# Kernel tuning notes

Measured on AMD Instinct MI355X. Metric: run time of the kernel, lower is better.

The kernel has to match this reference:

```python
import jax, jax.numpy as jnp
import numpy as np

HID = 1024
NH = 16
DH = HID // NH  # 64


def _heads(x):
    # [B, S, H] -> [B, nH, S, dh]
    B, S, _ = x.shape
    return x.reshape(B, S, NH, DH).transpose(0, 2, 1, 3)


def setup_inputs() -> dict:
    key = jax.random.key(0)
    ks = jax.random.split(key, 16)
    inp = {
        "word_hidden_states": jax.random.normal(ks[0], (2, 2048, HID), jnp.float32),
        "entity_hidden_states": jax.random.normal(ks[1], (2, 256, HID), jnp.float32),
    }
    scale = 1.0 / np.sqrt(HID)
    names = ["Wq", "Wk", "Wv", "Ww2e", "We2w", "We2e"]
    for i, n in enumerate(names):
        inp[n] = jax.random.normal(ks[2 + i], (HID, HID), jnp.float32) * scale
        inp["b" + n[1:]] = jnp.zeros((HID,), jnp.float32)
    return inp


def reference(word_hidden_states, entity_hidden_states,
              Wq, bq, Wk, bk, Wv, bv,
              Ww2e, bw2e, We2w, be2w, We2e, be2e):
    word, ent = word_hidden_states, entity_hidden_states
    B, Sw, _ = word.shape
    Se = ent.shape[1]
    hs = jnp.concatenate([word, ent], axis=1)  # [B, Sw+Se, H]

    # four query types, heads: [B, nH, S*, dh]
    q_w2w = _heads(word @ Wq + bq)
    q_w2e = _heads(word @ Ww2e + bw2e)
    q_e2w = _heads(ent @ We2w + be2w)
    q_e2e = _heads(ent @ We2e + be2e)

    k = _heads(hs @ Wk + bk)
    v = _heads(hs @ Wv + bv)
    k_w, k_e = k[:, :, :Sw, :], k[:, :, Sw:, :]

    # block scores
    s_w2w = jnp.einsum("bhqd,bhkd->bhqk", q_w2w, k_w)  # [B,nH,Sw,Sw]
    s_w2e = jnp.einsum("bhqd,bhkd->bhqk", q_w2e, k_e)  # [B,nH,Sw,Se]
    s_e2w = jnp.einsum("bhqd,bhkd->bhqk", q_e2w, k_w)  # [B,nH,Se,Sw]
    s_e2e = jnp.einsum("bhqd,bhkd->bhqk", q_e2e, k_e)  # [B,nH,Se,Se]

    word_scores = jnp.concatenate([s_w2w, s_w2e], axis=3)
    ent_scores = jnp.concatenate([s_e2w, s_e2e], axis=3)
    scores = jnp.concatenate([word_scores, ent_scores], axis=2)  # [B,nH,S,S]
    scores = scores / np.sqrt(DH)

    probs = jax.nn.softmax(scores, axis=-1)  # dropout is identity in eval
    ctx = jnp.einsum("bhqk,bhkd->bhqd", probs, v)  # [B,nH,S,dh]
    ctx = ctx.transpose(0, 2, 1, 3).reshape(B, Sw + Se, HID)
    return ctx[:, :Sw, :], ctx[:, Sw:, :]
```

## Files before the change

kernel.cpp:

```cpp
#include <hip/hip_runtime.h>
#include <hip/hip_bf16.h>

typedef __attribute__((ext_vector_type(8))) short short8;
typedef __attribute__((ext_vector_type(4))) float f32x4;
typedef __attribute__((ext_vector_type(16))) float f32x16;
typedef __attribute__((ext_vector_type(4))) unsigned short u16x4;
typedef __attribute__((ext_vector_type(8))) unsigned short u16x8;
typedef __attribute__((ext_vector_type(4))) unsigned int u32x4;

__device__ __forceinline__ unsigned short f2b(float f) {
  __hip_bfloat16 h = __float2bfloat16(f);
  return __builtin_bit_cast(unsigned short, h);
}

__device__ __forceinline__ float b2f(unsigned short u) {
  return __builtin_bit_cast(float, (unsigned int)u << 16);
}

__device__ __forceinline__ void gload_lds16(const void* g, void* l) {
  __builtin_amdgcn_global_load_lds(
      (const __attribute__((address_space(1))) unsigned int*)g,
      (__attribute__((address_space(3))) unsigned int*)l, 16, 0, 0);
}

__device__ __forceinline__ f32x16 mfma32(short8 a, short8 b, f32x16 c) {
  return __builtin_amdgcn_mfma_f32_32x32x16_bf16(a, b, c, 0, 0, 0);
}

__device__ __forceinline__ unsigned int cvtpk(float a, float b) {
  unsigned int r;
  asm("v_cvt_pk_bf16_f32 %0, %1, %2" : "=v"(r) : "v"(a), "v"(b));
  return r;
}

struct PrepassParams {
  const float* sw;
  const float* se;
  unsigned short* dw;
  unsigned short* de;
  const float* w[6];
  unsigned short* wt[6];
};

__global__ __launch_bounds__(256) void prepass(PrepassParams p) {
  const int bx = blockIdx.x;
  const int tid = threadIdx.x;
  if (bx < 2304) {
    int i = bx * 256 + tid;
    const float* s;
    unsigned short* d;
    int j;
    if (i < 524288) {
      s = p.sw; d = p.dw; j = i;
    } else {
      s = p.se; d = p.de; j = i - 524288;
      if (j >= 65536) return;
    }
    const f32x4* sp = (const f32x4*)s;
    f32x4 a = sp[2 * j];
    f32x4 b = sp[2 * j + 1];
    u16x8 o;
    o[0] = f2b(a[0]); o[1] = f2b(a[1]); o[2] = f2b(a[2]); o[3] = f2b(a[3]);
    o[4] = f2b(b[0]); o[5] = f2b(b[1]); o[6] = f2b(b[2]); o[7] = f2b(b[3]);
    ((u16x8*)d)[j] = o;
  } else {
    __shared__ float t[32][33];
    const int idx = bx - 2304;
    const int z = idx >> 10;
    const int rem = idx & 1023;
    const int bxx = rem & 31;
    const int byy = rem >> 5;
    const float* W = p.w[z];
    unsigned short* Wt = p.wt[z];
    const int tx = tid & 31, ty = tid >> 5;
#pragma unroll
    for (int i = 0; i < 4; ++i)
      t[ty + 8 * i][tx] = W[(byy * 32 + ty + 8 * i) * 1024 + bxx * 32 + tx];
    __syncthreads();
#pragma unroll
    for (int i = 0; i < 4; ++i)
      Wt[(bxx * 32 + ty + 8 * i) * 1024 + byy * 32 + tx] = f2b(t[tx][ty + 8 * i]);
  }
}

struct GemmJob {
  const unsigned short* Wt;
  const float* bias;
  unsigned short* out;
  int S;
  int s_off;
  int sshift;
  int trans;
  float scale;
};
struct Gemm2Params {
  const unsigned short* Aw;
  const unsigned short* Ae;
  GemmJob job[8];
};

__global__ __launch_bounds__(256) void gemm_qkv(Gemm2Params p) {
  __shared__ unsigned short smem[16384];
  unsigned short* As = smem;
  unsigned short* Bs = smem + 8192;
  const int tid = threadIdx.x;
  const int w = tid >> 6, lane = tid & 63;
  const int c = lane & 15, g = lane >> 4;
  const int wid = blockIdx.y + 36 * blockIdx.z;
  const int z = wid & 3;
  const int y = wid >> 2;
  const bool isword = y < 32;
  const GemmJob j = p.job[isword ? z : z + 4];
  const unsigned short* A = isword ? p.Aw : p.Ae;
  const long arow0 = (long)(isword ? y : y - 32) * 128;
  const unsigned short* B = j.Wt;
  const long brow0 = (long)blockIdx.x * 128;

  f32x4 acc[4][4] = {};

  for (int kt = 0; kt < 16; ++kt) {
    __syncthreads();
#pragma unroll
    for (int i = 0; i < 4; ++i) {
      int ch = i * 256 + tid;
      int row = ch >> 3;
      int k8 = ((ch & 7) ^ (row & 7)) << 3;
      const unsigned short* ga = A + (arow0 + row) * 1024 + kt * 64 + k8;
      const unsigned short* gb = B + (brow0 + row) * 1024 + kt * 64 + k8;
      gload_lds16(ga, As + (i * 256 + w * 64) * 8);
      gload_lds16(gb, Bs + (i * 256 + w * 64) * 8);
    }
    __syncthreads();
#pragma unroll
    for (int kf = 0; kf < 2; ++kf) {
      short8 av[4], bv[4];
#pragma unroll
      for (int mf = 0; mf < 4; ++mf) {
        int row = (w >> 1) * 64 + mf * 16 + c;
        int byte = (row * 128 + (kf * 32 + g * 8) * 2) ^ ((row & 7) << 4);
        av[mf] = *(const short8*)((const char*)As + byte);
      }
#pragma unroll
      for (int nf = 0; nf < 4; ++nf) {
        int row = (w & 1) * 64 + nf * 16 + c;
        int byte = (row * 128 + (kf * 32 + g * 8) * 2) ^ ((row & 7) << 4);
        bv[nf] = *(const short8*)((const char*)Bs + byte);
      }
      __builtin_amdgcn_s_setprio(1);
#pragma unroll
      for (int mf = 0; mf < 4; ++mf)
#pragma unroll
        for (int nf = 0; nf < 4; ++nf)
          acc[mf][nf] = __builtin_amdgcn_mfma_f32_16x16x32_bf16(av[mf], bv[nf],
                                                                acc[mf][nf], 0, 0, 0);
      __builtin_amdgcn_s_setprio(0);
    }
  }

  float biasv[4];
#pragma unroll
  for (int nf = 0; nf < 4; ++nf) {
    int n = (int)brow0 + (w & 1) * 64 + nf * 16 + c;
    biasv[nf] = j.bias[n];
  }
  const int smask = (1 << j.sshift) - 1;
  __syncthreads();

  if (j.trans) {
#pragma unroll
    for (int mf = 0; mf < 4; ++mf) {
      int m0 = (w >> 1) * 64 + mf * 16 + g * 4;
#pragma unroll
      for (int nf = 0; nf < 4; ++nf) {
        int n = (w & 1) * 64 + nf * 16 + c;
        u16x4 pv;
#pragma unroll
        for (int r = 0; r < 4; ++r)
          pv[r] = f2b((acc[mf][nf][r] + biasv[nf]) * j.scale);
        int byte = (n * 256 + m0 * 2) ^ ((n & 7) << 4);
        *(u16x4*)((char*)smem + byte) = pv;
      }
    }
    __syncthreads();
#pragma unroll
    for (int i = 0; i < 8; ++i) {
      int ch = i * 256 + tid;
      int nr = ch >> 4, sl = ch & 15;
      int byte = (nr * 256 + sl * 16) ^ ((nr & 7) << 4);
      u16x8 v = *(const u16x8*)((const char*)smem + byte);
      int n = (int)brow0 + nr;
      int hh = n >> 6, dd = n & 63;
      int m = (int)arow0 + sl * 8;
      int b_ = m >> j.sshift;
      int s = (m & smask) + j.s_off;
      *(u16x8*)(j.out + (((long)b_ * 16 + hh) * 64 + dd) * 2304 + s) = v;
    }
  } else {
#pragma unroll
    for (int mf = 0; mf < 4; ++mf) {
#pragma unroll
      for (int r = 0; r < 4; ++r) {
        int m = (w >> 1) * 64 + mf * 16 + g * 4 + r;
#pragma unroll
        for (int nf = 0; nf < 4; ++nf) {
          int n = (w & 1) * 64 + nf * 16 + c;
          unsigned short hv = f2b((acc[mf][nf][r] + biasv[nf]) * j.scale);
          int byte = (m * 256 + n * 2) ^ ((m & 7) << 4);
          *(unsigned short*)((char*)smem + byte) = hv;
        }
      }
    }
    __syncthreads();
#pragma unroll
    for (int i = 0; i < 8; ++i) {
      int ch = i * 256 + tid;
      int mr = ch >> 4, sl = ch & 15;
      int byte = (mr * 256 + sl * 16) ^ ((mr & 7) << 4);
      u16x8 v = *(const u16x8*)((const char*)smem + byte);
      int m = (int)arow0 + mr;
      int b_ = m >> j.sshift;
      int s = (m & smask) + j.s_off;
      int n = (int)brow0 + sl * 8;
      int hh = n >> 6, dd = n & 63;
      *(u16x8*)(j.out + (((long)b_ * 16 + hh) * j.S + s) * 64 + dd) = v;
    }
  }
}

__global__ __launch_bounds__(256) void attn_kernel(
    const unsigned short* __restrict__ qw2w, const unsigned short* __restrict__ qw2e,
    const unsigned short* __restrict__ qe2w, const unsigned short* __restrict__ qe2e,
    const unsigned short* __restrict__ Kg, const unsigned short* __restrict__ Vtg,
    unsigned short* __restrict__ po0, unsigned short* __restrict__ po1,
    float* __restrict__ lbuf) {
  __shared__ unsigned short smem[16384];

  const int tid = threadIdx.x;
  const int w = tid >> 6, lane = tid & 63;
  const int l31 = lane & 31, hf = lane >> 5;

  const int flat = blockIdx.x;
  const int work = (flat & 7) * 144 + (flat >> 3);
  const int part = work & 1;
  const int tile = (work % 36) >> 1;
  const int hb = work / 36;
  const int head = hb & 15, b = hb >> 4;

  const bool isw = tile < 16;
  const int Sq = isw ? 2048 : 256;
  const int q0 = (isw ? tile : tile - 16) * 128 + w * 32;
  const int bh = b * 16 + head;
  const unsigned short* Qa =
      (isw ? qw2w : qe2w) + ((long)bh * Sq + q0 + l31) * 64 + hf * 8;
  const unsigned short* Qb =
      (isw ? qw2e : qe2e) + ((long)bh * Sq + q0 + l31) * 64 + hf * 8;
  const unsigned short* Kb = Kg + (long)bh * 2304 * 64;
  const unsigned short* Vtb = Vtg + (long)bh * 64 * 2304;

  short8 qcur[4];
#pragma unroll
  for (int kf = 0; kf < 4; ++kf) qcur[kf] = *(const short8*)(Qa + kf * 16);

  f32x16 o[2] = {};
  float lrun = 0.f;

  auto stage = [&](int t, int bufi) {
    const unsigned short* Kt = Kb + t * 4096;
    unsigned short* Klp = smem + bufi * 4096;
    unsigned short* Vlp = smem + 8192 + bufi * 4096;
#pragma unroll
    for (int i = 0; i < 2; ++i) {
      int ch = i * 256 + tid;
      int row = ch >> 3, c8 = ch & 7;
      int col = (c8 ^ (row & 7)) << 3;
      gload_lds16(Kt + row * 64 + col, Klp + (i * 256 + (tid & 192)) * 8);
      gload_lds16(Vtb + row * 2304 + t * 64 + col, Vlp + (i * 256 + (tid & 192)) * 8);
    }
  };

  const int t0 = part * 18, t1 = t0 + 18;
  stage(t0, 0);
  int cur = 0;

  for (int t = t0; t < t1; ++t) {
    if (t == 32) {
#pragma unroll
      for (int kf = 0; kf < 4; ++kf) qcur[kf] = *(const short8*)(Qb + kf * 16);
    }
    if (t + 1 < t1) {
      stage(t + 1, cur ^ 1);
      asm volatile("s_waitcnt vmcnt(4)" ::: "memory");
    } else {
      asm volatile("s_waitcnt vmcnt(0)" ::: "memory");
    }
    __builtin_amdgcn_sched_barrier(0);
    __builtin_amdgcn_s_barrier();

    const char* Kbase = (const char*)(smem + cur * 4096);
    const char* Vbase = (const char*)(smem + 8192 + cur * 4096);

    f32x16 st[2] = {};
#pragma unroll
    for (int kg = 0; kg < 2; ++kg) {
      int row = kg * 32 + l31;
      int rb = (row * 128) | (hf * 16);
      int sw = (row & 7) << 4;
      short8 kfr[4];
#pragma unroll
      for (int kf = 0; kf < 4; ++kf)
        kfr[kf] = *(const short8*)(Kbase + ((rb + kf * 32) ^ sw));
      __builtin_amdgcn_s_setprio(1);
#pragma unroll
      for (int kf = 0; kf < 4; ++kf) st[kg] = mfma32(kfr[kf], qcur[kf], st[kg]);
      __builtin_amdgcn_s_setprio(0);
    }

    float s0 = 0.f, s1 = 0.f, s2 = 0.f, s3 = 0.f;
#pragma unroll
    for (int kg = 0; kg < 2; ++kg) {
#pragma unroll
      for (int r = 0; r < 16; r += 4) {
        float p0 = __builtin_amdgcn_exp2f(st[kg][r + 0]);
        float p1 = __builtin_amdgcn_exp2f(st[kg][r + 1]);
        float p2 = __builtin_amdgcn_exp2f(st[kg][r + 2]);
        float p3 = __builtin_amdgcn_exp2f(st[kg][r + 3]);
        st[kg][r + 0] = p0; st[kg][r + 1] = p1;
        st[kg][r + 2] = p2; st[kg][r + 3] = p3;
        s0 += p0; s1 += p1; s2 += p2; s3 += p3;
      }
    }
    lrun += (s0 + s1) + (s2 + s3);

#pragma unroll
    for (int kg = 0; kg < 2; ++kg)
#pragma unroll
      for (int hs = 0; hs < 2; ++hs) {
        const int rbase = hs * 8;
        unsigned int a0 = cvtpk(st[kg][rbase + 0], st[kg][rbase + 1]);
        unsigned int a1 = cvtpk(st[kg][rbase + 2], st[kg][rbase + 3]);
        unsigned int b0 = cvtpk(st[kg][rbase + 4], st[kg][rbase + 5]);
        unsigned int b1 = cvtpk(st[kg][rbase + 6], st[kg][rbase + 7]);
        asm("v_permlane32_swap_b32 %0, %1" : "+v"(a0), "+v"(b0));
        asm("v_permlane32_swap_b32 %0, %1" : "+v"(a1), "+v"(b1));
        u32x4 pw;
        pw[0] = a0; pw[1] = a1; pw[2] = b0; pw[3] = b1;
        short8 pf = __builtin_bit_cast(short8, pw);
        const int ks = kg * 2 + hs;
        short8 vf0, vf1;
        {
          int vrow = l31;
          int byte = ((vrow * 128) | (ks * 32 + hf * 16)) ^ ((vrow & 7) << 4);
          vf0 = *(const short8*)(Vbase + byte);
          vrow = 32 + l31;
          byte = ((vrow * 128) | (ks * 32 + hf * 16)) ^ ((vrow & 7) << 4);
          vf1 = *(const short8*)(Vbase + byte);
        }
        __builtin_amdgcn_s_setprio(1);
        o[0] = mfma32(vf0, pf, o[0]);
        o[1] = mfma32(vf1, pf, o[1]);
        __builtin_amdgcn_s_setprio(0);
      }

    asm volatile("s_waitcnt lgkmcnt(0)" ::: "memory");
    __builtin_amdgcn_sched_barrier(0);
    __builtin_amdgcn_s_barrier();
    cur ^= 1;
  }

  float ltot = lrun + __shfl_xor(lrun, 32);

  const int sgb = (isw ? 0 : 2048) + q0;
  if (hf == 0) lbuf[(long)part * 73728 + bh * 2304 + sgb + l31] = ltot;

  float* E = (float*)smem + w * 2048;
#pragma unroll
  for (int mf = 0; mf < 2; ++mf)
#pragma unroll
    for (int rg = 0; rg < 4; ++rg) {
      int d0 = mf * 32 + rg * 8 + hf * 4;
      f32x4 v;
      v[0] = o[mf][rg * 4 + 0];
      v[1] = o[mf][rg * 4 + 1];
      v[2] = o[mf][rg * 4 + 2];
      v[3] = o[mf][rg * 4 + 3];
      *(f32x4*)(E + l31 * 64 + (d0 ^ ((l31 & 7) << 2))) = v;
    }

  unsigned short* po = part ? po1 : po0;
  unsigned short* ob = isw
      ? po + (((long)b * 2048 + q0) * 1024 + head * 64)
      : po + (long)2 * 2048 * 1024 + (((long)b * 256 + q0) * 1024 + head * 64);
#pragma unroll
  for (int i = 0; i < 4; ++i) {
    int qr = (lane >> 3) + i * 8;
    int dcg = (lane & 7) * 8;
    int sw = (qr & 7) << 2;
    f32x4 v0 = *(const f32x4*)(E + qr * 64 + (dcg ^ sw));
    f32x4 v1 = *(const f32x4*)(E + qr * 64 + ((dcg + 4) ^ sw));
    u32x4 pk;
    pk[0] = cvtpk(v0[0], v0[1]);
    pk[1] = cvtpk(v0[2], v0[3]);
    pk[2] = cvtpk(v1[0], v1[1]);
    pk[3] = cvtpk(v1[2], v1[3]);
    *(u32x4*)(ob + (long)qr * 1024 + dcg) = pk;
  }
}

__global__ __launch_bounds__(256) void attn_merge(
    const unsigned short* __restrict__ po0, const unsigned short* __restrict__ po1,
    const float* __restrict__ lbuf, float* __restrict__ out) {
  long i = ((long)blockIdx.x * 256 + threadIdx.x) * 4;
  if (i >= 4718592) return;
  int bh, sg;
  if (i < 4194304) {
    int b = (int)(i >> 21), s = (int)((i >> 10) & 2047), h = (int)((i >> 6) & 15);
    bh = b * 16 + h;
    sg = s;
  } else {
    long j = i - 4194304;
    int b = (int)(j >> 18), s = (int)((j >> 10) & 255), h = (int)((j >> 6) & 15);
    bh = b * 16 + h;
    sg = 2048 + s;
  }
  float l0 = lbuf[bh * 2304 + sg];
  float l1 = lbuf[73728 + bh * 2304 + sg];
  u16x4 a4 = *(const u16x4*)(po0 + i);
  u16x4 c4 = *(const u16x4*)(po1 + i);
  float inv = 1.f / (l0 + l1);
  f32x4 r;
#pragma unroll
  for (int k = 0; k < 4; ++k) r[k] = (b2f(a4[k]) + b2f(c4[k])) * inv;
  *(f32x4*)(out + i) = r;
}

extern "C" void kernel_launch(void* const* d_in, const int* in_sizes, int n_in,
                              void* d_out, int out_size, void* d_ws, size_t ws_size,
                              hipStream_t stream) {
  (void)in_sizes; (void)n_in; (void)out_size; (void)ws_size;
  const float* word = (const float*)d_in[0];
  const float* ent = (const float*)d_in[1];

  char* ws = (char*)d_ws;
  size_t off = 0;
  auto alloc = [&](size_t bytes) {
    void* p = ws + off;
    off += (bytes + 255) & ~(size_t)255;
    return p;
  };
  unsigned short* Xw = (unsigned short*)alloc(4096ull * 1024 * 2);
  unsigned short* Xe = (unsigned short*)alloc(512ull * 1024 * 2);
  unsigned short* Wt[6];
  for (int i = 0; i < 6; ++i) Wt[i] = (unsigned short*)alloc(1024ull * 1024 * 2);
  unsigned short* qw2w = (unsigned short*)alloc(2ull * 16 * 2048 * 64 * 2);
  unsigned short* qw2e = (unsigned short*)alloc(2ull * 16 * 2048 * 64 * 2);
  unsigned short* qe2w = (unsigned short*)alloc(2ull * 16 * 256 * 64 * 2);
  unsigned short* qe2e = (unsigned short*)alloc(2ull * 16 * 256 * 64 * 2);
  unsigned short* Kbuf = (unsigned short*)alloc(2ull * 16 * 2304 * 64 * 2);
  unsigned short* Vtbuf = (unsigned short*)alloc(2ull * 16 * 64 * 2304 * 2);
  unsigned short* po1 = (unsigned short*)alloc(4718592ull * 2);
  float* lbuf = (float*)alloc(2ull * 73728 * 4);
  unsigned short* po0 = (unsigned short*)ws;

  PrepassParams pp;
  pp.sw = word;
  pp.se = ent;
  pp.dw = Xw;
  pp.de = Xe;
  pp.w[0] = (const float*)d_in[2];
  pp.w[1] = (const float*)d_in[4];
  pp.w[2] = (const float*)d_in[6];
  pp.w[3] = (const float*)d_in[8];
  pp.w[4] = (const float*)d_in[10];
  pp.w[5] = (const float*)d_in[12];
  for (int i = 0; i < 6; ++i) pp.wt[i] = Wt[i];
  prepass<<<8448, 256, 0, stream>>>(pp);

  const float* bq = (const float*)d_in[3];
  const float* bk = (const float*)d_in[5];
  const float* bv = (const float*)d_in[7];
  const float* bw2e = (const float*)d_in[9];
  const float* be2w = (const float*)d_in[11];
  const float* be2e = (const float*)d_in[13];
  const float qs = 0.125f * 1.44269504f;

  Gemm2Params gp;
  gp.Aw = Xw;
  gp.Ae = Xe;
  gp.job[0] = {Wt[0], bq, qw2w, 2048, 0, 11, 0, qs};
  gp.job[1] = {Wt[3], bw2e, qw2e, 2048, 0, 11, 0, qs};
  gp.job[2] = {Wt[1], bk, Kbuf, 2304, 0, 11, 0, 1.f};
  gp.job[3] = {Wt[2], bv, Vtbuf, 2304, 0, 11, 1, 1.f};
  gp.job[4] = {Wt[4], be2w, qe2w, 256, 0, 8, 0, qs};
  gp.job[5] = {Wt[5], be2e, qe2e, 256, 0, 8, 0, qs};
  gp.job[6] = {Wt[1], bk, Kbuf, 2304, 2048, 8, 0, 1.f};
  gp.job[7] = {Wt[2], bv, Vtbuf, 2304, 2048, 8, 1, 1.f};
  gemm_qkv<<<dim3(8, 36, 4), 256, 0, stream>>>(gp);

  attn_kernel<<<1152, 256, 0, stream>>>(qw2w, qw2e, qe2w, qe2e, Kbuf, Vtbuf,
                                        po0, po1, lbuf);
  attn_merge<<<4608, 256, 0, stream>>>(po0, po1, lbuf, (float*)d_out);
}
```

Before: 141.6 us.

## Fuse split-KV merge into attention kernel via per-pair atomic counter

```diff
diff --git a/kernel.cpp b/kernel.cpp
--- a/kernel.cpp
+++ b/kernel.cpp
@@ -40,11 +40,15 @@
   unsigned short* de;
   const float* w[6];
   unsigned short* wt[6];
+  int* cnt;
 };
 
 __global__ __launch_bounds__(256) void prepass(PrepassParams p) {
   const int bx = blockIdx.x;
   const int tid = threadIdx.x;
+  if (bx == 8447) {
+    for (int k = tid; k < 576; k += 256) p.cnt[k] = 0;
+  }
   if (bx < 2304) {
     int i = bx * 256 + tid;
     const float* s;
@@ -232,7 +236,7 @@
     const unsigned short* __restrict__ qe2w, const unsigned short* __restrict__ qe2e,
     const unsigned short* __restrict__ Kg, const unsigned short* __restrict__ Vtg,
     unsigned short* __restrict__ po0, unsigned short* __restrict__ po1,
-    float* __restrict__ lbuf) {
+    float* __restrict__ lbuf, int* __restrict__ cnt, float* __restrict__ out) {
   __shared__ unsigned short smem[16384];
 
   const int tid = threadIdx.x;
@@ -242,6 +246,7 @@
   const int flat = blockIdx.x;
   const int work = (flat & 7) * 144 + (flat >> 3);
   const int part = work & 1;
+  const int pair = work >> 1;
   const int tile = (work % 36) >> 1;
   const int hb = work / 36;
   const int head = hb & 15, b = hb >> 4;
@@ -386,10 +391,11 @@
       *(f32x4*)(E + l31 * 64 + (d0 ^ ((l31 & 7) << 2))) = v;
     }
 
-  unsigned short* po = part ? po1 : po0;
-  unsigned short* ob = isw
-      ? po + (((long)b * 2048 + q0) * 1024 + head * 64)
-      : po + (long)2 * 2048 * 1024 + (((long)b * 256 + q0) * 1024 + head * 64);
+  unsigned short* pself = part ? po1 : po0;
+  const long obase = isw ? (((long)b * 2048 + q0) * 1024 + head * 64)
+                         : (long)2 * 2048 * 1024 +
+                               (((long)b * 256 + q0) * 1024 + head * 64);
+  unsigned short* obs = pself + obase;
 #pragma unroll
   for (int i = 0; i < 4; ++i) {
     int qr = (lane >> 3) + i * 8;
@@ -402,35 +408,38 @@
     pk[1] = cvtpk(v0[2], v0[3]);
     pk[2] = cvtpk(v1[0], v1[1]);
     pk[3] = cvtpk(v1[2], v1[3]);
-    *(u32x4*)(ob + (long)qr * 1024 + dcg) = pk;
-  }
-}
-
-__global__ __launch_bounds__(256) void attn_merge(
-    const unsigned short* __restrict__ po0, const unsigned short* __restrict__ po1,
-    const float* __restrict__ lbuf, float* __restrict__ out) {
-  long i = ((long)blockIdx.x * 256 + threadIdx.x) * 4;
-  if (i >= 4718592) return;
-  int bh, sg;
-  if (i < 4194304) {
-    int b = (int)(i >> 21), s = (int)((i >> 10) & 2047), h = (int)((i >> 6) & 15);
-    bh = b * 16 + h;
-    sg = s;
-  } else {
-    long j = i - 4194304;
-    int b = (int)(j >> 18), s = (int)((j >> 10) & 255), h = (int)((j >> 6) & 15);
-    bh = b * 16 + h;
-    sg = 2048 + s;
-  }
-  float l0 = lbuf[bh * 2304 + sg];
-  float l1 = lbuf[73728 + bh * 2304 + sg];
-  u16x4 a4 = *(const u16x4*)(po0 + i);
-  u16x4 c4 = *(const u16x4*)(po1 + i);
-  float inv = 1.f / (l0 + l1);
-  f32x4 r;
-#pragma unroll
-  for (int k = 0; k < 4; ++k) r[k] = (b2f(a4[k]) + b2f(c4[k])) * inv;
-  *(f32x4*)(out + i) = r;
+    *(u32x4*)(obs + (long)qr * 1024 + dcg) = pk;
+  }
+
+  __threadfence();
+  __syncthreads();
+  __shared__ int flagLds;
+  if (tid == 0) flagLds = atomicAdd(&cnt[pair], 1);
+  __syncthreads();
+  if (flagLds == 1) {
+    const unsigned short* pother = part ? po0 : po1;
+    const unsigned short* obo = pother + obase;
+    float* oo = out + obase;
+    const float* lb0 = lbuf + bh * 2304 + sgb;
+    const float* lb1 = lbuf + 73728 + bh * 2304 + sgb;
+#pragma unroll
+    for (int i = 0; i < 4; ++i) {
+      int qr = (lane >> 3) + i * 8;
+      int dcg = (lane & 7) * 8;
+      long off = (long)qr * 1024 + dcg;
+      u16x8 a8 = *(const u16x8*)(obs + off);
+      u16x8 b8 = *(const u16x8*)(obo + off);
+      float inv = 1.f / (lb0[qr] + lb1[qr]);
+      f32x4 r0, r1;
+#pragma unroll
+      for (int k = 0; k < 4; ++k) {
+        r0[k] = (b2f(a8[k]) + b2f(b8[k])) * inv;
+        r1[k] = (b2f(a8[4 + k]) + b2f(b8[4 + k])) * inv;
+      }
+      *(f32x4*)(oo + off) = r0;
+      *(f32x4*)(oo + off + 4) = r1;
+    }
+  }
 }
 
 extern "C" void kernel_launch(void* const* d_in, const int* in_sizes, int n_in,
@@ -457,9 +466,10 @@
   unsigned short* qe2e = (unsigned short*)alloc(2ull * 16 * 256 * 64 * 2);
   unsigned short* Kbuf = (unsigned short*)alloc(2ull * 16 * 2304 * 64 * 2);
   unsigned short* Vtbuf = (unsigned short*)alloc(2ull * 16 * 64 * 2304 * 2);
+  unsigned short* po0 = (unsigned short*)alloc(4718592ull * 2);
   unsigned short* po1 = (unsigned short*)alloc(4718592ull * 2);
   float* lbuf = (float*)alloc(2ull * 73728 * 4);
-  unsigned short* po0 = (unsigned short*)ws;
+  int* cnt = (int*)alloc(576 * 4);
 
   PrepassParams pp;
   pp.sw = word;
@@ -473,6 +483,7 @@
   pp.w[4] = (const float*)d_in[10];
   pp.w[5] = (const float*)d_in[12];
   for (int i = 0; i < 6; ++i) pp.wt[i] = Wt[i];
+  pp.cnt = cnt;
   prepass<<<8448, 256, 0, stream>>>(pp);
 
   const float* bq = (const float*)d_in[3];
@@ -497,6 +508,5 @@
   gemm_qkv<<<dim3(8, 36, 4), 256, 0, stream>>>(gp);
 
   attn_kernel<<<1152, 256, 0, stream>>>(qw2w, qw2e, qe2w, qe2e, Kbuf, Vtbuf,
-                                        po0, po1, lbuf);
-  attn_merge<<<4608, 256, 0, stream>>>(po0, po1, lbuf, (float*)d_out);
-}
+                                        po0, po1, lbuf, cnt, (float*)d_out);
+}
```

Result: slower. 260.5 us (+84.0%).
